# Performance work log

Hardware: AMD Instinct MI355X
Metric: run time of the kernel (lower is better)

## Reference

```python
import jax, jax.numpy as jnp
import numpy as np

N_NODES, N_VARS, E = 100000, 50000, 640000
FEAT, H, L = 16, 128, 4
N_INT, K = 20000, 8  # integer vars with categorical heads, uniform domain size


def _mlp2(x, W1, b1, W2, b2):
    return jnp.maximum(x @ W1 + b1, 0.0) @ W2 + b2


def setup_inputs() -> dict:
    key = jax.random.key(0)
    ks = jax.random.split(key, 24)
    s = lambda i, shape, scale: jax.random.normal(ks[i], shape, dtype=jnp.float32) * scale
    inp = {
        "x": jax.random.normal(ks[0], (N_NODES, FEAT), dtype=jnp.float32),
        "edge_index": jax.random.randint(ks[1], (2, E), 0, N_NODES, dtype=jnp.int32).astype(jnp.int64),
        "num_vars": N_VARS,
        # NodeEmbedder (var / cons)
        "ve_W1": s(2, (FEAT, H), 0.25), "ve_b1": jnp.zeros((H,), jnp.float32),
        "ve_W2": s(3, (H, H), 0.09),   "ve_b2": jnp.zeros((H,), jnp.float32),
        "ce_W1": s(4, (FEAT, H), 0.25), "ce_b1": jnp.zeros((H,), jnp.float32),
        "ce_W2": s(5, (H, H), 0.09),   "ce_b2": jnp.zeros((H,), jnp.float32),
        # GCN backbone: stacked per-layer params
        "conv_W": s(6, (L, H, H), 0.09), "conv_b": jnp.zeros((L, H), jnp.float32),
        "ref_W1": s(7, (L, H, H), 0.09), "ref_b1": jnp.zeros((L, H), jnp.float32),
        "ref_W2": s(8, (L, H, H), 0.09), "ref_b2": jnp.zeros((L, H), jnp.float32),
        # Bernoulli head: H -> H//2 -> 1
        "bh_W1": s(9, (H, H // 2), 0.09), "bh_b1": jnp.zeros((H // 2,), jnp.float32),
        "bh_W2": s(10, (H // 2, 1), 0.12), "bh_b2": jnp.zeros((1,), jnp.float32),
        # Categorical heads: one Linear(H, K) per integer variable, batched
        "cat_W": s(11, (N_INT, H, K), 0.09),
        "cat_b": jnp.zeros((N_INT, K), jnp.float32),
    }
    return inp


def reference(x, edge_index, num_vars,
              ve_W1, ve_b1, ve_W2, ve_b2,
              ce_W1, ce_b1, ce_W2, ce_b2,
              conv_W, conv_b, ref_W1, ref_b1, ref_W2, ref_b2,
              bh_W1, bh_b1, bh_W2, bh_b2,
              cat_W, cat_b):
    N = x.shape[0]
    src, dst = edge_index[0], edge_index[1]
    # GCN normalization with self-loops: deg includes the self edge
    deg = jax.ops.segment_sum(jnp.ones((src.shape[0],), x.dtype), dst, num_segments=N) + 1.0
    dinv_sqrt = jax.lax.rsqrt(deg)
    enorm = dinv_sqrt[src] * dinv_sqrt[dst]      # [E]
    self_norm = (1.0 / deg)[:, None]             # [N,1] self-loop weight deg^-1

    var_h = _mlp2(x[:num_vars], ve_W1, ve_b1, ve_W2, ve_b2)
    cons_h = _mlp2(x[num_vars:], ce_W1, ce_b1, ce_W2, ce_b2)
    h = jnp.concatenate([var_h, cons_h], axis=0)  # [N,H]

    def gcn_conv(xin, W, b):
        hw = xin @ W
        agg = jax.ops.segment_sum(hw[src] * enorm[:, None], dst, num_segments=N)
        return agg + hw * self_norm + b

    def layer(xc, p):
        W, b, W1, b1, W2, b2 = p
        h_ = jnp.maximum(gcn_conv(xc, W, b), 0.0)
        return xc + _mlp2(h_, W1, b1, W2, b2), None

    h, _ = jax.lax.scan(layer, h, (conv_W, conv_b, ref_W1, ref_b1, ref_W2, ref_b2))

    vh = h[:num_vars]
    bern_logits = _mlp2(vh, bh_W1, bh_b1, bh_W2, bh_b2)[:, 0]          # [num_vars]
    n_int = cat_W.shape[0]
    cat_logits = jnp.einsum('nh,nhk->nk', vh[:n_int], cat_W) + cat_b    # [n_int,K]
    return bern_logits, cat_logits
```

## Files before the change

kernel.cpp:

```cpp
#include <hip/hip_runtime.h>
#include <hip/hip_bf16.h>

#define NN 100000
#define NV 50000
#define NE 640000
#define FEAT 16
#define HD 128
#define NL 4
#define NI 20000
#define KK 8
#define NPB 16
#define SCAN_BLK 98
#define LDP 136

typedef __hip_bfloat16 bf16;
typedef __attribute__((ext_vector_type(8))) short short8;
typedef __attribute__((ext_vector_type(4))) float f32x4;

static __device__ __forceinline__ ushort f2bu(float f) {
    __hip_bfloat16 b = __float2bfloat16(f);
    return *reinterpret_cast<ushort*>(&b);
}
static __device__ __forceinline__ float bu2f(ushort u) {
    __hip_bfloat16 b = *reinterpret_cast<__hip_bfloat16*>(&u);
    return __bfloat162float(b);
}

__global__ void k_deg_init(float* deg) {
    int i = blockIdx.x * blockDim.x + threadIdx.x;
    if (i < NN) deg[i] = 1.0f;
}

__global__ void k_deg_scatter(const int* __restrict__ ei, float* deg) {
    int e = blockIdx.x * blockDim.x + threadIdx.x;
    if (e < NE) atomicAdd(&deg[ei[NE + e]], 1.0f);
}

__global__ void k_deg_fin(const float* __restrict__ deg, float* dinv, float* selfn) {
    int i = blockIdx.x * blockDim.x + threadIdx.x;
    if (i < NN) {
        float d = deg[i];
        dinv[i]  = rsqrtf(d);
        selfn[i] = 1.0f / d;
    }
}

__global__ void k_scan_part(const float* __restrict__ deg, int* __restrict__ part) {
    __shared__ int s[256];
    const int t = threadIdx.x;
    const int i = blockIdx.x * 1024 + t * 4;
    int sum = 0;
#pragma unroll
    for (int j = 0; j < 4; ++j)
        if (i + j < NN) sum += (int)deg[i + j] - 1;
    s[t] = sum;
    __syncthreads();
    for (int off = 128; off > 0; off >>= 1) {
        if (t < off) s[t] += s[t + off];
        __syncthreads();
    }
    if (t == 0) part[blockIdx.x] = s[0];
}

__global__ void k_scan_mid(const int* __restrict__ part, int* __restrict__ blockoff,
                           int* __restrict__ row_ptr) {
    __shared__ int s[128];
    const int t = threadIdx.x;
    int v = (t < SCAN_BLK) ? part[t] : 0;
    s[t] = v;
    __syncthreads();
    for (int off = 1; off < 128; off <<= 1) {
        int u = (t >= off) ? s[t - off] : 0;
        __syncthreads();
        s[t] += u;
        __syncthreads();
    }
    if (t < SCAN_BLK) blockoff[t] = s[t] - v;
    if (t == 0) row_ptr[NN] = NE;
}

__global__ void k_scan_apply(const float* __restrict__ deg,
                             const int* __restrict__ blockoff,
                             int* __restrict__ row_ptr, int* __restrict__ cnt) {
    __shared__ int s[256];
    const int t = threadIdx.x;
    const int i = blockIdx.x * 1024 + t * 4;
    int c[4];
    int tsum = 0;
#pragma unroll
    for (int j = 0; j < 4; ++j) {
        c[j] = (i + j < NN) ? (int)deg[i + j] - 1 : 0;
        tsum += c[j];
    }
    s[t] = tsum;
    __syncthreads();
    for (int off = 1; off < 256; off <<= 1) {
        int u = (t >= off) ? s[t - off] : 0;
        __syncthreads();
        s[t] += u;
        __syncthreads();
    }
    int off = blockoff[blockIdx.x] + s[t] - tsum;
#pragma unroll
    for (int j = 0; j < 4; ++j) {
        if (i + j < NN) {
            row_ptr[i + j] = off;
            cnt[i + j] = 0;
            off += c[j];
        }
    }
}

__global__ void k_csr_fill(const int* __restrict__ ei,
                           const int* __restrict__ row_ptr, int* __restrict__ cnt,
                           const float* __restrict__ dinv,
                           int* __restrict__ col, float* __restrict__ wgt) {
    int e = blockIdx.x * blockDim.x + threadIdx.x;
    if (e >= NE) return;
    const int s = ei[e];
    const int d = ei[NE + e];
    const int pos = row_ptr[d] + atomicAdd(&cnt[d], 1);
    col[pos] = s;
    wgt[pos] = dinv[s] * dinv[d];
}

__global__ void k_wprep(const float* __restrict__ conv_W,
                        const float* __restrict__ ref_W1,
                        const float* __restrict__ ref_W2,
                        ushort* __restrict__ wt) {
    const int mat = blockIdx.x >> 7;
    const int j = blockIdx.x & 127;
    const int k = threadIdx.x;
    const float* src = (mat < 4) ? conv_W + (size_t)mat * HD * HD
                     : (mat < 8) ? ref_W1 + (size_t)(mat - 4) * HD * HD
                                 : ref_W2 + (size_t)(mat - 8) * HD * HD;
    wt[(size_t)mat * HD * HD + j * HD + k] = f2bu(src[k * HD + j]);
}

__global__ __launch_bounds__(HD) void k_embed(
                        const float* __restrict__ x,
                        const float* __restrict__ vW1, const float* __restrict__ vb1,
                        const float* __restrict__ vW2, const float* __restrict__ vb2,
                        const float* __restrict__ cW1, const float* __restrict__ cb1,
                        const float* __restrict__ cW2, const float* __restrict__ cb2,
                        float* __restrict__ h, ushort* __restrict__ hb) {
    const int j = threadIdx.x;
    const int n0 = blockIdx.x * NPB;
    __shared__ float xs[NPB][FEAT];
    __shared__ float hid[NPB][HD];

    const float *W1, *b1, *W2, *b2;
    if (n0 < NV) { W1 = vW1; b1 = vb1; W2 = vW2; b2 = vb2; }
    else         { W1 = cW1; b1 = cb1; W2 = cW2; b2 = cb2; }

    xs[j >> 4][j & 15] = x[(size_t)n0 * FEAT + j];
    xs[8 + (j >> 4)][j & 15] = x[(size_t)n0 * FEAT + 128 + j];
    __syncthreads();

    float acc[NPB];
    const float bb1 = b1[j];
#pragma unroll
    for (int m = 0; m < NPB; ++m) acc[m] = bb1;
#pragma unroll
    for (int f = 0; f < FEAT; ++f) {
        const float w = W1[f * HD + j];
#pragma unroll
        for (int m = 0; m < NPB; ++m) acc[m] += xs[m][f] * w;
    }
#pragma unroll
    for (int m = 0; m < NPB; ++m) hid[m][j] = fmaxf(acc[m], 0.0f);
    __syncthreads();

    const float bb2 = b2[j];
#pragma unroll
    for (int m = 0; m < NPB; ++m) acc[m] = bb2;
#pragma unroll 8
    for (int k = 0; k < HD; ++k) {
        const float w = W2[k * HD + j];
#pragma unroll
        for (int m = 0; m < NPB; ++m) acc[m] += hid[m][k] * w;
    }
#pragma unroll
    for (int m = 0; m < NPB; ++m) {
        h[(size_t)(n0 + m) * HD + j] = acc[m];
        hb[(size_t)(n0 + m) * HD + j] = f2bu(acc[m]);
    }
}

__global__ __launch_bounds__(256) void k_hw(
                     const ushort* __restrict__ hb, const ushort* __restrict__ Wt,
                     ushort* __restrict__ hwb) {
    const int lane = threadIdx.x & 63;
    const int w = threadIdx.x >> 6;
    const int row0 = blockIdx.x * 128 + w * 32;
    const int l15 = lane & 15, lg = lane >> 4;

    const f32x4 zero = {0.f, 0.f, 0.f, 0.f};
    f32x4 acc[2][8];
#pragma unroll
    for (int rt = 0; rt < 2; ++rt)
#pragma unroll
        for (int jt = 0; jt < 8; ++jt) acc[rt][jt] = zero;

#pragma unroll
    for (int ks = 0; ks < 4; ++ks) {
        short8 a[2];
#pragma unroll
        for (int rt = 0; rt < 2; ++rt) {
            int r = row0 + rt * 16 + l15;
            r = r < NN ? r : NN - 1;
            a[rt] = *reinterpret_cast<const short8*>(&hb[(size_t)r * HD + ks * 32 + lg * 8]);
        }
#pragma unroll
        for (int jt = 0; jt < 8; ++jt) {
            short8 b = *reinterpret_cast<const short8*>(&Wt[(jt * 16 + l15) * HD + ks * 32 + lg * 8]);
            acc[0][jt] = __builtin_amdgcn_mfma_f32_16x16x32_bf16(a[0], b, acc[0][jt], 0, 0, 0);
            acc[1][jt] = __builtin_amdgcn_mfma_f32_16x16x32_bf16(a[1], b, acc[1][jt], 0, 0, 0);
        }
    }
#pragma unroll
    for (int rt = 0; rt < 2; ++rt)
#pragma unroll
        for (int jt = 0; jt < 8; ++jt)
#pragma unroll
            for (int r = 0; r < 4; ++r) {
                int row = row0 + rt * 16 + lg * 4 + r;
                if (row < NN) hwb[(size_t)row * HD + jt * 16 + l15] = f2bu(acc[rt][jt][r]);
            }
}

__global__ __launch_bounds__(512, 4) void k_combine(
                          const ushort* __restrict__ hwb,
                          const int* __restrict__ row_ptr,
                          const int* __restrict__ col,
                          const float* __restrict__ wgt,
                          const float* __restrict__ selfn,
                          const float* __restrict__ cb,
                          const ushort* __restrict__ Wt1, const float* __restrict__ b1,
                          const ushort* __restrict__ Wt2, const float* __restrict__ b2,
                          float* __restrict__ h, ushort* __restrict__ hb) {
    const int t = threadIdx.x;
    const int n0 = blockIdx.x * 64;
    __shared__ ushort hs[64][LDP];
    __shared__ ushort hid[64][LDP];
    __shared__ int rp[65];

    if (t <= 64) {
        int idx = n0 + t;
        rp[t] = row_ptr[idx < NN ? idx : NN];
    }
    __syncthreads();

    const int lane = t & 63, w = t >> 6;
    {
        const int c0 = 2 * lane;
        const float cbx = cb[c0], cby = cb[c0 + 1];
        float accx[8], accy[8];
        int ecur[8], eend[8];
        int rounds = 0;
#pragma unroll
        for (int m = 0; m < 8; ++m) {
            const int node = n0 + w * 8 + m;
            const int nc = node < NN ? node : NN - 1;
            const uint hv = *reinterpret_cast<const uint*>(&hwb[(size_t)nc * HD + c0]);
            const float sn = selfn[nc];
            accx[m] = bu2f((ushort)(hv & 0xffffu)) * sn + cbx;
            accy[m] = bu2f((ushort)(hv >> 16)) * sn + cby;
            ecur[m] = rp[w * 8 + m];
            eend[m] = rp[w * 8 + m + 1];
            rounds = max(rounds, eend[m] - ecur[m]);
        }
#pragma unroll 1
        for (int r = 0; r < rounds; r += 2) {
            uint va[8], vb[8];
            float wa[8], wb[8];
            int ca[8], cc[8];
#pragma unroll
            for (int m = 0; m < 8; ++m) {
                const int e0 = ecur[m];
                const int a0 = (e0 < eend[m]) ? e0 : 0;
                const int a1 = (e0 + 1 < eend[m]) ? e0 + 1 : 0;
                wa[m] = (e0 < eend[m]) ? wgt[a0] : 0.0f;
                wb[m] = (e0 + 1 < eend[m]) ? wgt[a1] : 0.0f;
                ca[m] = col[a0];
                cc[m] = col[a1];
            }
#pragma unroll
            for (int m = 0; m < 8; ++m) {
                va[m] = *reinterpret_cast<const uint*>(&hwb[(size_t)ca[m] * HD + c0]);
                vb[m] = *reinterpret_cast<const uint*>(&hwb[(size_t)cc[m] * HD + c0]);
            }
#pragma unroll
            for (int m = 0; m < 8; ++m) {
                accx[m] += wa[m] * bu2f((ushort)(va[m] & 0xffffu));
                accy[m] += wa[m] * bu2f((ushort)(va[m] >> 16));
                accx[m] += wb[m] * bu2f((ushort)(vb[m] & 0xffffu));
                accy[m] += wb[m] * bu2f((ushort)(vb[m] >> 16));
            }
#pragma unroll
            for (int m = 0; m < 8; ++m) ecur[m] += 2;
        }
#pragma unroll
        for (int m = 0; m < 8; ++m) {
            const uint px = (uint)f2bu(fmaxf(accx[m], 0.0f));
            const uint py = (uint)f2bu(fmaxf(accy[m], 0.0f));
            *reinterpret_cast<uint*>(&hs[w * 8 + m][c0]) = px | (py << 16);
        }
    }
    __syncthreads();

    const int l15 = lane & 15, lg = lane >> 4;
    const int rt = (w & 3) * 16;
    const int c0 = (w >> 2) * 64;

    f32x4 acc1[4];
#pragma unroll
    for (int jt = 0; jt < 4; ++jt) {
        float bv = b1[c0 + jt * 16 + l15];
        f32x4 v = {bv, bv, bv, bv};
        acc1[jt] = v;
    }
#pragma unroll
    for (int ks = 0; ks < 4; ++ks) {
        short8 a = *reinterpret_cast<const short8*>(&hs[rt + l15][ks * 32 + lg * 8]);
#pragma unroll
        for (int jt = 0; jt < 4; ++jt) {
            short8 b = *reinterpret_cast<const short8*>(&Wt1[(c0 + jt * 16 + l15) * HD + ks * 32 + lg * 8]);
            acc1[jt] = __builtin_amdgcn_mfma_f32_16x16x32_bf16(a, b, acc1[jt], 0, 0, 0);
        }
    }
#pragma unroll
    for (int jt = 0; jt < 4; ++jt)
#pragma unroll
        for (int r = 0; r < 4; ++r)
            hid[rt + lg * 4 + r][c0 + jt * 16 + l15] = f2bu(fmaxf(acc1[jt][r], 0.0f));
    __syncthreads();

    f32x4 acc2[4];
#pragma unroll
    for (int jt = 0; jt < 4; ++jt) {
        float bv = b2[c0 + jt * 16 + l15];
        f32x4 v = {bv, bv, bv, bv};
        acc2[jt] = v;
    }
#pragma unroll
    for (int ks = 0; ks < 4; ++ks) {
        short8 a = *reinterpret_cast<const short8*>(&hid[rt + l15][ks * 32 + lg * 8]);
#pragma unroll
        for (int jt = 0; jt < 4; ++jt) {
            short8 b = *reinterpret_cast<const short8*>(&Wt2[(c0 + jt * 16 + l15) * HD + ks * 32 + lg * 8]);
            acc2[jt] = __builtin_amdgcn_mfma_f32_16x16x32_bf16(a, b, acc2[jt], 0, 0, 0);
        }
    }
#pragma unroll
    for (int jt = 0; jt < 4; ++jt)
#pragma unroll
        for (int r = 0; r < 4; ++r) {
            const int row = n0 + rt + lg * 4 + r;
            if (row < NN) {
                const size_t idx = (size_t)row * HD + c0 + jt * 16 + l15;
                const float v = acc2[jt][r] + h[idx];
                h[idx] = v;
                hb[idx] = f2bu(v);
            }
        }
}

__global__ void k_bern(const float* __restrict__ h,
                       const float* __restrict__ W1, const float* __restrict__ b1,
                       const float* __restrict__ W2, const float* __restrict__ b2,
                       float* __restrict__ out) {
    const long long t = (long long)blockIdx.x * blockDim.x + threadIdx.x;
    const int n = (int)(t >> 6);
    const int lane = (int)(t & 63);
    if (n >= NV) return;
    const float* hn = h + (size_t)n * HD;
    float acc = b1[lane];
#pragma unroll 8
    for (int k = 0; k < HD; ++k) acc += hn[k] * W1[k * 64 + lane];
    float p = fmaxf(acc, 0.0f) * W2[lane];
#pragma unroll
    for (int off = 32; off > 0; off >>= 1) p += __shfl_down(p, off);
    if (lane == 0) out[n] = p + b2[0];
}

__global__ void k_cat(const float* __restrict__ h,
                      const float* __restrict__ cW, const float* __restrict__ cb,
                      float* __restrict__ out) {
    const long long t = (long long)blockIdx.x * blockDim.x + threadIdx.x;
    const int n = (int)(t >> 6);
    const int lane = (int)(t & 63);
    if (n >= NI) return;
    const float* hn = h + (size_t)n * HD;
    float p[KK];
#pragma unroll
    for (int k = 0; k < KK; ++k) p[k] = 0.0f;
#pragma unroll
    for (int half = 0; half < 2; ++half) {
        const int hh = lane + 64 * half;
        const float vh = hn[hh];
        const float* wp = cW + ((size_t)n * HD + hh) * KK;
#pragma unroll
        for (int k = 0; k < KK; ++k) p[k] += vh * wp[k];
    }
#pragma unroll
    for (int k = 0; k < KK; ++k) {
#pragma unroll
        for (int off = 32; off > 0; off >>= 1) p[k] += __shfl_down(p[k], off);
    }
    if (lane == 0) {
#pragma unroll
        for (int k = 0; k < KK; ++k) out[NV + (size_t)n * KK + k] = p[k] + cb[(size_t)n * KK + k];
    }
}

extern "C" void kernel_launch(void* const* d_in, const int* in_sizes, int n_in,
                              void* d_out, int out_size, void* d_ws, size_t ws_size,
                              hipStream_t stream) {
    const float* x  = (const float*)d_in[0];
    const int*   ei = (const int*)d_in[1];
    const float* ve_W1 = (const float*)d_in[3];
    const float* ve_b1 = (const float*)d_in[4];
    const float* ve_W2 = (const float*)d_in[5];
    const float* ve_b2 = (const float*)d_in[6];
    const float* ce_W1 = (const float*)d_in[7];
    const float* ce_b1 = (const float*)d_in[8];
    const float* ce_W2 = (const float*)d_in[9];
    const float* ce_b2 = (const float*)d_in[10];
    const float* conv_W = (const float*)d_in[11];
    const float* conv_b = (const float*)d_in[12];
    const float* ref_W1 = (const float*)d_in[13];
    const float* ref_b1 = (const float*)d_in[14];
    const float* ref_W2 = (const float*)d_in[15];
    const float* ref_b2 = (const float*)d_in[16];
    const float* bh_W1 = (const float*)d_in[17];
    const float* bh_b1 = (const float*)d_in[18];
    const float* bh_W2 = (const float*)d_in[19];
    const float* bh_b2 = (const float*)d_in[20];
    const float* cat_W = (const float*)d_in[21];
    const float* cat_b = (const float*)d_in[22];
    float* out = (float*)d_out;

    const size_t need = (size_t)(3 * NN + (NN + 1) + NN + 2 * NE + 2 * SCAN_BLK) * 4
                      + (size_t)NN * HD * 4
                      + (size_t)NN * HD * 2
                      + (size_t)NN * HD * 2
                      + (size_t)12 * HD * HD * 2;
    if (ws_size < need) return;

    float* deg     = (float*)d_ws;
    float* dinv    = deg + NN;
    float* selfn   = dinv + NN;
    int*   row_ptr = (int*)(selfn + NN);
    int*   cnt     = row_ptr + (NN + 1);
    int*   col     = cnt + NN;
    float* wgt     = (float*)(col + NE);
    int*   part    = (int*)(wgt + NE);
    int*   blockoff= part + SCAN_BLK;
    float* h       = (float*)(blockoff + SCAN_BLK);
    ushort* hwb    = (ushort*)(h + (size_t)NN * HD);
    ushort* hb     = hwb + (size_t)NN * HD;
    ushort* wt     = hb + (size_t)NN * HD;

    k_deg_init<<<(NN + 255) / 256, 256, 0, stream>>>(deg);
    k_deg_scatter<<<(NE + 255) / 256, 256, 0, stream>>>(ei, deg);
    k_deg_fin<<<(NN + 255) / 256, 256, 0, stream>>>(deg, dinv, selfn);
    k_scan_part<<<SCAN_BLK, 256, 0, stream>>>(deg, part);
    k_scan_mid<<<1, 128, 0, stream>>>(part, blockoff, row_ptr);
    k_scan_apply<<<SCAN_BLK, 256, 0, stream>>>(deg, blockoff, row_ptr, cnt);
    k_csr_fill<<<(NE + 255) / 256, 256, 0, stream>>>(ei, row_ptr, cnt, dinv, col, wgt);
    k_wprep<<<12 * 128, 128, 0, stream>>>(conv_W, ref_W1, ref_W2, wt);

    k_embed<<<NN / NPB, HD, 0, stream>>>(x, ve_W1, ve_b1, ve_W2, ve_b2,
                                         ce_W1, ce_b1, ce_W2, ce_b2, h, hb);

    for (int l = 0; l < NL; ++l) {
        k_hw<<<(NN + 127) / 128, 256, 0, stream>>>(hb, wt + (size_t)l * HD * HD, hwb);
        k_combine<<<(NN + 63) / 64, 512, 0, stream>>>(hwb, row_ptr, col, wgt, selfn,
                                               conv_b + (size_t)l * HD,
                                               wt + (size_t)(4 + l) * HD * HD,
                                               ref_b1 + (size_t)l * HD,
                                               wt + (size_t)(8 + l) * HD * HD,
                                               ref_b2 + (size_t)l * HD,
                                               h, hb);
    }

    k_bern<<<(NV * 64) / 256, 256, 0, stream>>>(h, bh_W1, bh_b1, bh_W2, bh_b2, out);
    k_cat<<<(NI * 64) / 256, 256, 0, stream>>>(h, cat_W, cat_b, out);
}
```

Before: 921.4 us.

## Rewrite node embedding MLP with bf16 MFMA and pre-transposed weights

Replaces the scalar fp32 embedding MLP with a bf16 MFMA kernel that tiles 128 nodes per block. The intermediate hidden layer is staged in LDS, and the first layer's K dimension is padded to 32. A small prep kernel transposes and converts the embedder weights to bf16. Variable and constraint nodes are launched separately. This reduces ALU-bound embedding cost, but the embedding is now computed at bf16 precision.

```diff
diff --git a/kernel.cpp b/kernel.cpp
--- a/kernel.cpp
+++ b/kernel.cpp
@@ -9,9 +9,9 @@
 #define NL 4
 #define NI 20000
 #define KK 8
-#define NPB 16
 #define SCAN_BLK 98
 #define LDP 136
+#define WE_STRIDE (128*32 + 128*128)
 
 typedef __hip_bfloat16 bf16;
 typedef __attribute__((ext_vector_type(8))) short short8;
@@ -137,53 +137,83 @@
     wt[(size_t)mat * HD * HD + j * HD + k] = f2bu(src[k * HD + j]);
 }
 
-__global__ __launch_bounds__(HD) void k_embed(
-                        const float* __restrict__ x,
-                        const float* __restrict__ vW1, const float* __restrict__ vb1,
-                        const float* __restrict__ vW2, const float* __restrict__ vb2,
-                        const float* __restrict__ cW1, const float* __restrict__ cb1,
-                        const float* __restrict__ cW2, const float* __restrict__ cb2,
-                        float* __restrict__ h, ushort* __restrict__ hb) {
-    const int j = threadIdx.x;
-    const int n0 = blockIdx.x * NPB;
-    __shared__ float xs[NPB][FEAT];
-    __shared__ float hid[NPB][HD];
-
-    const float *W1, *b1, *W2, *b2;
-    if (n0 < NV) { W1 = vW1; b1 = vb1; W2 = vW2; b2 = vb2; }
-    else         { W1 = cW1; b1 = cb1; W2 = cW2; b2 = cb2; }
-
-    xs[j >> 4][j & 15] = x[(size_t)n0 * FEAT + j];
-    xs[8 + (j >> 4)][j & 15] = x[(size_t)n0 * FEAT + 128 + j];
-    __syncthreads();
-
-    float acc[NPB];
-    const float bb1 = b1[j];
-#pragma unroll
-    for (int m = 0; m < NPB; ++m) acc[m] = bb1;
-#pragma unroll
-    for (int f = 0; f < FEAT; ++f) {
-        const float w = W1[f * HD + j];
-#pragma unroll
-        for (int m = 0; m < NPB; ++m) acc[m] += xs[m][f] * w;
-    }
-#pragma unroll
-    for (int m = 0; m < NPB; ++m) hid[m][j] = fmaxf(acc[m], 0.0f);
-    __syncthreads();
-
-    const float bb2 = b2[j];
-#pragma unroll
-    for (int m = 0; m < NPB; ++m) acc[m] = bb2;
-#pragma unroll 8
-    for (int k = 0; k < HD; ++k) {
-        const float w = W2[k * HD + j];
-#pragma unroll
-        for (int m = 0; m < NPB; ++m) acc[m] += hid[m][k] * w;
-    }
-#pragma unroll
-    for (int m = 0; m < NPB; ++m) {
-        h[(size_t)(n0 + m) * HD + j] = acc[m];
-        hb[(size_t)(n0 + m) * HD + j] = f2bu(acc[m]);
+__global__ void k_wprep_embed(const float* __restrict__ vW1, const float* __restrict__ vW2,
+                              const float* __restrict__ cW1, const float* __restrict__ cW2,
+                              ushort* __restrict__ wte) {
+    const int side = blockIdx.x >> 7;
+    const int j = blockIdx.x & 127;
+    const int k = threadIdx.x;
+    const float* W1 = side ? cW1 : vW1;
+    const float* W2 = side ? cW2 : vW2;
+    ushort* o = wte + (size_t)side * WE_STRIDE;
+    if (k < 32) o[j * 32 + k] = (k < FEAT) ? f2bu(W1[k * HD + j]) : (ushort)0;
+    o[128 * 32 + j * HD + k] = f2bu(W2[k * HD + j]);
+}
+
+__global__ __launch_bounds__(256, 4) void k_embed_mfma(
+        const float* __restrict__ x,
+        const ushort* __restrict__ W1t, const float* __restrict__ b1,
+        const ushort* __restrict__ W2t, const float* __restrict__ b2,
+        int nbase, int nend,
+        float* __restrict__ h, ushort* __restrict__ hb) {
+    const int lane = threadIdx.x & 63, w = threadIdx.x >> 6;
+    const int l15 = lane & 15, lg = lane >> 4;
+    const int rowb = nbase + blockIdx.x * 128;
+    __shared__ ushort hsm[128][LDP];
+
+#pragma unroll
+    for (int rt = 0; rt < 2; ++rt) {
+        const int r = rowb + w * 32 + rt * 16 + l15;
+        const int rc = r < nend ? r : nend - 1;
+        short8 a = {0, 0, 0, 0, 0, 0, 0, 0};
+        if (lg < 2) {
+            const float* xp = x + (size_t)rc * FEAT + lg * 8;
+#pragma unroll
+            for (int i = 0; i < 8; ++i) a[i] = (short)f2bu(xp[i]);
+        }
+#pragma unroll
+        for (int jt = 0; jt < 8; ++jt) {
+            const float bv = b1[jt * 16 + l15];
+            f32x4 acc = {bv, bv, bv, bv};
+            short8 b = *reinterpret_cast<const short8*>(&W1t[(jt * 16 + l15) * 32 + lg * 8]);
+            acc = __builtin_amdgcn_mfma_f32_16x16x32_bf16(a, b, acc, 0, 0, 0);
+#pragma unroll
+            for (int rr = 0; rr < 4; ++rr)
+                hsm[w * 32 + rt * 16 + lg * 4 + rr][jt * 16 + l15] =
+                    f2bu(fmaxf(acc[rr], 0.0f));
+        }
+    }
+    __syncthreads();
+
+#pragma unroll
+    for (int rt = 0; rt < 2; ++rt) {
+        f32x4 acc[8];
+#pragma unroll
+        for (int jt = 0; jt < 8; ++jt) {
+            const float bv = b2[jt * 16 + l15];
+            f32x4 v = {bv, bv, bv, bv};
+            acc[jt] = v;
+        }
+#pragma unroll
+        for (int ks = 0; ks < 4; ++ks) {
+            short8 a = *reinterpret_cast<const short8*>(&hsm[w * 32 + rt * 16 + l15][ks * 32 + lg * 8]);
+#pragma unroll
+            for (int jt = 0; jt < 8; ++jt) {
+                short8 b = *reinterpret_cast<const short8*>(&W2t[(jt * 16 + l15) * HD + ks * 32 + lg * 8]);
+                acc[jt] = __builtin_amdgcn_mfma_f32_16x16x32_bf16(a, b, acc[jt], 0, 0, 0);
+            }
+        }
+#pragma unroll
+        for (int jt = 0; jt < 8; ++jt)
+#pragma unroll
+            for (int rr = 0; rr < 4; ++rr) {
+                const int row = rowb + w * 32 + rt * 16 + lg * 4 + rr;
+                if (row < nend) {
+                    const size_t idx = (size_t)row * HD + jt * 16 + l15;
+                    h[idx] = acc[jt][rr];
+                    hb[idx] = f2bu(acc[jt][rr]);
+                }
+            }
     }
 }
 
@@ -445,7 +475,8 @@
                       + (size_t)NN * HD * 4
                       + (size_t)NN * HD * 2
                       + (size_t)NN * HD * 2
-                      + (size_t)12 * HD * HD * 2;
+                      + (size_t)12 * HD * HD * 2
+                      + (size_t)2 * WE_STRIDE * 2;
     if (ws_size < need) return;
 
     float* deg     = (float*)d_ws;
@@ -461,6 +492,7 @@
     ushort* hwb    = (ushort*)(h + (size_t)NN * HD);
     ushort* hb     = hwb + (size_t)NN * HD;
     ushort* wt     = hb + (size_t)NN * HD;
+    ushort* wte    = wt + (size_t)12 * HD * HD;
 
     k_deg_init<<<(NN + 255) / 256, 256, 0, stream>>>(deg);
     k_deg_scatter<<<(NE + 255) / 256, 256, 0, stream>>>(ei, deg);
@@ -470,9 +502,12 @@
     k_scan_apply<<<SCAN_BLK, 256, 0, stream>>>(deg, blockoff, row_ptr, cnt);
     k_csr_fill<<<(NE + 255) / 256, 256, 0, stream>>>(ei, row_ptr, cnt, dinv, col, wgt);
     k_wprep<<<12 * 128, 128, 0, stream>>>(conv_W, ref_W1, ref_W2, wt);
-
-    k_embed<<<NN / NPB, HD, 0, stream>>>(x, ve_W1, ve_b1, ve_W2, ve_b2,
-                                         ce_W1, ce_b1, ce_W2, ce_b2, h, hb);
+    k_wprep_embed<<<256, 128, 0, stream>>>(ve_W1, ve_W2, ce_W1, ce_W2, wte);
+
+    k_embed_mfma<<<(NV + 127) / 128, 256, 0, stream>>>(
+        x, wte, ve_b1, wte + 128 * 32, ve_b2, 0, NV, h, hb);
+    k_embed_mfma<<<(NN - NV + 127) / 128, 256, 0, stream>>>(
+        x, wte + WE_STRIDE, ce_b1, wte + WE_STRIDE + 128 * 32, ce_b2, NV, NN, h, hb);
 
     for (int l = 0; l < NL; ++l) {
         k_hw<<<(NN + 127) / 128, 256, 0, stream>>>(hb, wt + (size_t)l * HD * HD, hwb);
```

Result: faster. 854.1 us (-7.3%).
